# Optimization experiments

Hardware: AMD Instinct MI355X
Metric: run time of the kernel (lower is better)

The kernel has to match this reference:

```python
import jax, jax.numpy as jnp
import numpy as np

N = 100000          # total nodes
F = 128             # in_features
B = 1000            # number of graphs
NPG = 100           # nodes per graph (contiguous)
DEG = 16            # avg degree
E = B * NPG * DEG   # total edges (intra-graph)
K_RATIO = 0.8
KNUM = max(1, int(K_RATIO * NPG))  # nodes kept per graph = 80


def setup_inputs() -> dict:
    key = jax.random.key(0)
    k1, k2, k3, k4 = jax.random.split(key, 4)
    x = jax.random.normal(k1, (N, F), dtype=jnp.float32)
    # intra-graph random edges: offset each block of NPG*DEG edges by its graph's base node id
    offs = (jnp.arange(E, dtype=jnp.int32) // (NPG * DEG)) * NPG
    src = jax.random.randint(k2, (E,), 0, NPG, dtype=jnp.int32) + offs
    dst = jax.random.randint(k3, (E,), 0, NPG, dtype=jnp.int32) + offs
    edge_index = jnp.stack([src, dst], axis=0)
    batch = (jnp.arange(N, dtype=jnp.int32) // NPG).astype(jnp.int32)
    limit = float(np.sqrt(6.0 / (F + 1)))  # xavier_uniform for (F,1)
    theta_att = jax.random.uniform(k4, (F, 1), dtype=jnp.float32, minval=-limit, maxval=limit)
    return {"x": x, "edge_index": edge_index, "batch": batch, "theta_att": theta_att}


def reference(x, edge_index, batch, theta_att):
    num_nodes = x.shape[0]
    # add self loops with weight 1
    loops = jnp.arange(num_nodes, dtype=edge_index.dtype)
    row = jnp.concatenate([edge_index[0], loops])
    col = jnp.concatenate([edge_index[1], loops])
    w = jnp.ones(row.shape[0], dtype=x.dtype)
    # symmetric degree normalization (degree counted over row, as in torch code)
    deg = jax.ops.segment_sum(w, row, num_segments=num_nodes)
    dis = jnp.where(deg > 0, jax.lax.rsqrt(deg), jnp.zeros((), x.dtype))
    norm = dis[row] * w * dis[col]
    # scatter-add: agg[dst] += x[src] * norm
    agg = jax.ops.segment_sum(x[row] * norm[:, None], col, num_segments=num_nodes)
    z = (agg @ theta_att)[:, 0]                     # (N,)
    # per-graph top-k: graphs are contiguous and equal-sized -> reshape
    zb = z.reshape(B, NPG)
    _, pos = jax.lax.top_k(zb, KNUM)                # (B, KNUM) positions within each graph
    pos = jnp.sort(pos, axis=1)                     # global sort of keep_idx == per-graph sort here
    keep = (pos + jnp.arange(B, dtype=pos.dtype)[:, None] * NPG).reshape(-1)  # (B*KNUM,)
    scale = jax.nn.sigmoid(z[keep])[:, None]
    x_new = x[keep] * scale                         # (B*KNUM, F)
    batch_new = batch[keep]
    # subgraph with relabeled nodes; dropped edges padded with -1 (fixed shape for jit)
    node_mask = jnp.zeros(num_nodes, dtype=bool).at[keep].set(True)
    new_id = jnp.cumsum(node_mask.astype(jnp.int32)) - 1
    emask = node_mask[edge_index[0]] & node_mask[edge_index[1]]
    edge_index_new = jnp.where(emask[None, :], new_id[edge_index], -1)
    return x_new, edge_index_new, batch_new
```

## Files before the change

### kernel.cpp

```cpp
#include <hip/hip_runtime.h>


#define NPG   100
#define EPG   1600
#define KNUM  80
#define FDIM  128
#define BT    512
#define GPB   2
#define NF4   (NPG * FDIM / 4)
#define NE4   (EPG / 4)
#define NCH   (NF4 / BT)
#define NREM  (NF4 - NCH * BT)
#define PSTR  33

struct Smem {
    int4   edge4[NE4];
    int    cnt[8][NPG];
    double part[NPG * PSTR];
    double dis[NPG];
    double a[NPG];
    double zp[8][NPG];
    double z[NPG];
    unsigned long long mask7[8];
    int    newid[NPG];
    float  scalen[NPG];
};

__device__ __forceinline__
void process_graph(Smem& sm, int g, int tid, int wave, int lane, float4 th,
                   const float4 (&v)[NCH], float4 vR, int4 es, int4 ed,
                   float* __restrict__ out, int E_total, int out_x_elems)
{
    const int  base = g * NPG;
    const bool hasE = tid < NE4;
    const bool hasR = tid < NREM;
    int* sh_edge = (int*)sm.edge4;

    {
        int*    cw = sm.cnt[wave];
        double* zw = sm.zp[wave];
        for (int i = lane; i < NPG; i += 64) { cw[i] = 0; zw[i] = 0.0; }
    }

    int4 p;
    if (hasE) {
        int4 s4 = es, d4 = ed;
        s4.x -= base; s4.y -= base; s4.z -= base; s4.w -= base;
        d4.x -= base; d4.y -= base; d4.z -= base; d4.w -= base;
        p.x = s4.x | (d4.x << 16); p.y = s4.y | (d4.y << 16);
        p.z = s4.z | (d4.z << 16); p.w = s4.w | (d4.w << 16);
        sm.edge4[tid] = p;
        int* cw = sm.cnt[wave];
        atomicAdd(&cw[s4.x], 1); atomicAdd(&cw[s4.y], 1);
        atomicAdd(&cw[s4.z], 1); atomicAdd(&cw[s4.w], 1);
    }

    #pragma unroll
    for (int i = 0; i < NCH; ++i) {
        int idx = i * BT + tid;
        double dp = (double)v[i].x * th.x + (double)v[i].y * th.y
                  + (double)v[i].z * th.z + (double)v[i].w * th.w;
        sm.part[idx + (idx >> 5)] = dp;
    }
    if (hasR) {
        int idx = NCH * BT + tid;
        double dp = (double)vR.x * th.x + (double)vR.y * th.y
                  + (double)vR.z * th.z + (double)vR.w * th.w;
        sm.part[idx + (idx >> 5)] = dp;
    }
    __syncthreads();

    if (tid < 4 * NPG) {
        const int n = tid >> 2, q = tid & 3;
        const double* pr = sm.part + n * PSTR + q * 8;
        double s = ((pr[0] + pr[1]) + (pr[2] + pr[3]))
                 + ((pr[4] + pr[5]) + (pr[6] + pr[7]));
        s += __shfl_xor(s, 1, 64);
        s += __shfl_xor(s, 2, 64);
        if (q == 0) {
            int deg = 1 + sm.cnt[0][n] + sm.cnt[1][n] + sm.cnt[2][n]
                        + sm.cnt[3][n] + sm.cnt[4][n] + sm.cnt[5][n]
                        + sm.cnt[6][n] + sm.cnt[7][n];
            double dis = 1.0 / sqrt((double)deg);
            sm.dis[n] = dis;
            sm.a[n]   = s * dis;
        }
    }
    __syncthreads();

    {
        double* zw = sm.zp[wave];
        for (int j = tid; j < EPG; j += BT) {
            int e = sh_edge[j];
            atomicAdd(&zw[e >> 16], sm.a[e & 0xffff]);
        }
    }
    __syncthreads();

    if (tid < NPG) {
        double zi = sm.a[tid]
                  + sm.zp[0][tid] + sm.zp[1][tid] + sm.zp[2][tid] + sm.zp[3][tid]
                  + sm.zp[4][tid] + sm.zp[5][tid] + sm.zp[6][tid] + sm.zp[7][tid];
        sm.z[tid] = zi * sm.dis[tid];
        sm.newid[tid] = -1;
    }
    __syncthreads();

    const bool rk = tid < 4 * NPG;
    const int  n2 = tid >> 2;
    int r = 0;
    double zn = 0.0;
    if (rk) {
        zn = sm.z[n2];
        const int j0 = (tid & 3) * 25;
        for (int j = j0; j < j0 + 25; ++j) {
            double zj = sm.z[j];
            r += (int)((zj > zn) | ((zj == zn) & (j < n2)));
        }
    }
    r += __shfl_xor(r, 1, 64);
    r += __shfl_xor(r, 2, 64);
    const bool lead = rk && ((tid & 3) == 0) && (r < KNUM);
    unsigned long long m = __ballot(lead);
    if (lane == 0) sm.mask7[wave] = m;
    __syncthreads();

    if (lead) {
        int before = __popcll(m & ((1ull << lane) - 1ull));
        for (int w2 = 0; w2 < wave; ++w2) before += __popcll(sm.mask7[w2]);
        int row = g * KNUM + before;
        sm.newid[n2]  = row;
        sm.scalen[n2] = 1.0f / (1.0f + __expf(-(float)zn));
        out[(size_t)out_x_elems + 2 * (size_t)E_total + row] = (float)g;
    }
    __syncthreads();

    float4* outx = (float4*)out;
    #pragma unroll
    for (int i = 0; i < NCH; ++i) {
        int idx = i * BT + tid;
        int nid = sm.newid[idx >> 5];
        if (nid >= 0) {
            float sc = sm.scalen[idx >> 5];
            float4 o;
            o.x = v[i].x * sc; o.y = v[i].y * sc;
            o.z = v[i].z * sc; o.w = v[i].w * sc;
            outx[(size_t)nid * 32 + (idx & 31)] = o;
        }
    }
    if (hasR) {
        int idx = NCH * BT + tid;
        int nid = sm.newid[idx >> 5];
        if (nid >= 0) {
            float sc = sm.scalen[idx >> 5];
            float4 o;
            o.x = vR.x * sc; o.y = vR.y * sc;
            o.z = vR.z * sc; o.w = vR.w * sc;
            outx[(size_t)nid * 32 + (idx & 31)] = o;
        }
    }

    float* e0 = out + out_x_elems;
    float* e1 = e0 + E_total;
    if (hasE) {
        float4 o0, o1;
        {
            int a_ = sm.newid[p.x & 0xffff], b_ = sm.newid[p.x >> 16];
            bool vv = (a_ >= 0) && (b_ >= 0);
            o0.x = vv ? (float)a_ : -1.0f; o1.x = vv ? (float)b_ : -1.0f;
        }
        {
            int a_ = sm.newid[p.y & 0xffff], b_ = sm.newid[p.y >> 16];
            bool vv = (a_ >= 0) && (b_ >= 0);
            o0.y = vv ? (float)a_ : -1.0f; o1.y = vv ? (float)b_ : -1.0f;
        }
        {
            int a_ = sm.newid[p.z & 0xffff], b_ = sm.newid[p.z >> 16];
            bool vv = (a_ >= 0) && (b_ >= 0);
            o0.z = vv ? (float)a_ : -1.0f; o1.z = vv ? (float)b_ : -1.0f;
        }
        {
            int a_ = sm.newid[p.w & 0xffff], b_ = sm.newid[p.w >> 16];
            bool vv = (a_ >= 0) && (b_ >= 0);
            o0.w = vv ? (float)a_ : -1.0f; o1.w = vv ? (float)b_ : -1.0f;
        }
        ((float4*)e0)[(size_t)g * NE4 + tid] = o0;
        ((float4*)e1)[(size_t)g * NE4 + tid] = o1;
    }
}

__global__ __launch_bounds__(BT, 4)
void sagpool_fused7(const float* __restrict__ x,
                    const int*   __restrict__ ei,
                    const float* __restrict__ theta,
                    float* __restrict__ out,
                    int E_total, int out_x_elems, int n_graphs)
{
    __shared__ Smem sm;
    const int tid  = threadIdx.x;
    const int wave = tid >> 6;
    const int lane = tid & 63;
    const int gA   = blockIdx.x * GPB;
    const int gB   = gA + 1;
    const bool hasE = tid < NE4;
    const bool hasR = tid < NREM;

    const float4 th = ((const float4*)theta)[lane & 31];

    int4 esA, edA, esB, edB;
    float4 vA[NCH], vB[NCH], vRA, vRB;

    if (hasE) {
        esA = ((const int4*)(ei + (size_t)gA * EPG))[tid];
        edA = ((const int4*)(ei + (size_t)E_total + (size_t)gA * EPG))[tid];
    }
    {
        const float4* xb4 = (const float4*)(x + (size_t)gA * NPG * FDIM);
        #pragma unroll
        for (int i = 0; i < NCH; ++i) vA[i] = xb4[i * BT + tid];
        if (hasR) vRA = xb4[NCH * BT + tid];
    }
    const bool doB = gB < n_graphs;
    if (doB) {
        if (hasE) {
            esB = ((const int4*)(ei + (size_t)gB * EPG))[tid];
            edB = ((const int4*)(ei + (size_t)E_total + (size_t)gB * EPG))[tid];
        }
        const float4* xb4 = (const float4*)(x + (size_t)gB * NPG * FDIM);
        #pragma unroll
        for (int i = 0; i < NCH; ++i) vB[i] = xb4[i * BT + tid];
        if (hasR) vRB = xb4[NCH * BT + tid];
    }

    process_graph(sm, gA, tid, wave, lane, th, vA, vRA, esA, edA,
                  out, E_total, out_x_elems);
    if (doB)
        process_graph(sm, gB, tid, wave, lane, th, vB, vRB, esB, edB,
                      out, E_total, out_x_elems);
}

extern "C" void kernel_launch(void* const* d_in, const int* in_sizes, int n_in,
                              void* d_out, int out_size, void* d_ws, size_t ws_size,
                              hipStream_t stream)
{
    const float* x     = (const float*)d_in[0];
    const int*   ei    = (const int*)d_in[1];
    const float* theta = (const float*)d_in[3];
    float* out = (float*)d_out;

    const int N = in_sizes[0] / FDIM;
    const int E = in_sizes[1] / 2;
    const int B = N / NPG;
    const int out_x_elems = B * KNUM * FDIM;
    const int nb = (B + GPB - 1) / GPB;

    sagpool_fused7<<<dim3(nb), dim3(BT), 0, stream>>>(x, ei, theta, out,
                                                      E, out_x_elems, B);
}
```

Before: 129.7 us.

## Prefetch second graph's features into LDS via async global_load_lds during first graph

Instead of holding both graphs' feature rows in registers, the kernel keeps only graph A in registers and streams graph B's features directly into a 51KB LDS buffer with global_load_lds while graph A is processed. The per-node dot-product partials are pre-reduced with lane shuffles, shrinking the partial array and the reduction step. Barriers are replaced with a variant that waits only on LDS counters so the async prefetch is not drained at each sync. This cuts register pressure but raises LDS use per block, which may reduce occupancy. The prefetch also relies on the barrier before graph B to make the global_load_lds data visible.

```diff
diff --git a/kernel.cpp b/kernel.cpp
--- a/kernel.cpp
+++ b/kernel.cpp
@@ -6,17 +6,17 @@
 #define KNUM  80
 #define FDIM  128
 #define BT    512
-#define GPB   2
 #define NF4   (NPG * FDIM / 4)
 #define NE4   (EPG / 4)
 #define NCH   (NF4 / BT)
 #define NREM  (NF4 - NCH * BT)
-#define PSTR  33
+#define P8    9
 
 struct Smem {
+    alignas(16) float xB[NPG * FDIM];
     int4   edge4[NE4];
     int    cnt[8][NPG];
-    double part[NPG * PSTR];
+    double part[NPG * P8];
     double dis[NPG];
     double a[NPG];
     double zp[8][NPG];
@@ -26,9 +26,20 @@
     float  scalen[NPG];
 };
 
+typedef __attribute__((address_space(1))) const unsigned int gu32;
+typedef __attribute__((address_space(3))) unsigned int lu32;
+
+__device__ __forceinline__ void bar_nodrain() {
+    asm volatile("s_waitcnt lgkmcnt(0)" ::: "memory");
+    __builtin_amdgcn_s_barrier();
+    asm volatile("" ::: "memory");
+}
+
+template<bool FROMLDS, bool PF>
 __device__ __forceinline__
 void process_graph(Smem& sm, int g, int tid, int wave, int lane, float4 th,
-                   const float4 (&v)[NCH], float4 vR, int4 es, int4 ed,
+                   float4 (&v)[NCH], float4& vR, int4 es, int4 ed,
+                   const float4* pfsrc,
                    float* __restrict__ out, int E_total, int out_x_elems)
 {
     const int  base = g * NPG;
@@ -55,38 +66,56 @@
         atomicAdd(&cw[s4.z], 1); atomicAdd(&cw[s4.w], 1);
     }
 
+    const float4* xl = (const float4*)sm.xB;
     #pragma unroll
     for (int i = 0; i < NCH; ++i) {
         int idx = i * BT + tid;
+        if (FROMLDS) v[i] = xl[idx];
         double dp = (double)v[i].x * th.x + (double)v[i].y * th.y
                   + (double)v[i].z * th.z + (double)v[i].w * th.w;
-        sm.part[idx + (idx >> 5)] = dp;
+        dp += __shfl_xor(dp, 1, 64);
+        dp += __shfl_xor(dp, 2, 64);
+        if ((lane & 3) == 0)
+            sm.part[(idx >> 5) * P8 + ((idx & 31) >> 2)] = dp;
     }
     if (hasR) {
         int idx = NCH * BT + tid;
+        if (FROMLDS) vR = xl[idx];
         double dp = (double)vR.x * th.x + (double)vR.y * th.y
                   + (double)vR.z * th.z + (double)vR.w * th.w;
-        sm.part[idx + (idx >> 5)] = dp;
-    }
-    __syncthreads();
-
-    if (tid < 4 * NPG) {
-        const int n = tid >> 2, q = tid & 3;
-        const double* pr = sm.part + n * PSTR + q * 8;
+        dp += __shfl_xor(dp, 1, 64);
+        dp += __shfl_xor(dp, 2, 64);
+        if ((lane & 3) == 0)
+            sm.part[(idx >> 5) * P8 + ((idx & 31) >> 2)] = dp;
+    }
+
+    if (PF) {
+        #pragma unroll
+        for (int i = 0; i < NCH; ++i) {
+            int idx = i * BT + tid;
+            __builtin_amdgcn_global_load_lds((gu32*)(pfsrc + idx),
+                (lu32*)(sm.xB + (size_t)(i * BT + wave * 64) * 4), 16, 0, 0);
+        }
+        if (wave < 2) {
+            int idx = NCH * BT + tid;
+            __builtin_amdgcn_global_load_lds((gu32*)(pfsrc + idx),
+                (lu32*)(sm.xB + (size_t)(NCH * BT + wave * 64) * 4), 16, 0, 0);
+        }
+    }
+    bar_nodrain();
+
+    if (tid < NPG) {
+        const double* pr = sm.part + tid * P8;
         double s = ((pr[0] + pr[1]) + (pr[2] + pr[3]))
                  + ((pr[4] + pr[5]) + (pr[6] + pr[7]));
-        s += __shfl_xor(s, 1, 64);
-        s += __shfl_xor(s, 2, 64);
-        if (q == 0) {
-            int deg = 1 + sm.cnt[0][n] + sm.cnt[1][n] + sm.cnt[2][n]
-                        + sm.cnt[3][n] + sm.cnt[4][n] + sm.cnt[5][n]
-                        + sm.cnt[6][n] + sm.cnt[7][n];
-            double dis = 1.0 / sqrt((double)deg);
-            sm.dis[n] = dis;
-            sm.a[n]   = s * dis;
-        }
-    }
-    __syncthreads();
+        int deg = 1 + sm.cnt[0][tid] + sm.cnt[1][tid] + sm.cnt[2][tid]
+                    + sm.cnt[3][tid] + sm.cnt[4][tid] + sm.cnt[5][tid]
+                    + sm.cnt[6][tid] + sm.cnt[7][tid];
+        double dis = 1.0 / sqrt((double)deg);
+        sm.dis[tid] = dis;
+        sm.a[tid]   = s * dis;
+    }
+    bar_nodrain();
 
     {
         double* zw = sm.zp[wave];
@@ -95,7 +124,7 @@
             atomicAdd(&zw[e >> 16], sm.a[e & 0xffff]);
         }
     }
-    __syncthreads();
+    bar_nodrain();
 
     if (tid < NPG) {
         double zi = sm.a[tid]
@@ -104,7 +133,7 @@
         sm.z[tid] = zi * sm.dis[tid];
         sm.newid[tid] = -1;
     }
-    __syncthreads();
+    bar_nodrain();
 
     const bool rk = tid < 4 * NPG;
     const int  n2 = tid >> 2;
@@ -123,7 +152,7 @@
     const bool lead = rk && ((tid & 3) == 0) && (r < KNUM);
     unsigned long long m = __ballot(lead);
     if (lane == 0) sm.mask7[wave] = m;
-    __syncthreads();
+    bar_nodrain();
 
     if (lead) {
         int before = __popcll(m & ((1ull << lane) - 1ull));
@@ -133,7 +162,7 @@
         sm.scalen[n2] = 1.0f / (1.0f + __expf(-(float)zn));
         out[(size_t)out_x_elems + 2 * (size_t)E_total + row] = (float)g;
     }
-    __syncthreads();
+    bar_nodrain();
 
     float4* outx = (float4*)out;
     #pragma unroll
@@ -190,7 +219,7 @@
 }
 
 __global__ __launch_bounds__(BT, 4)
-void sagpool_fused7(const float* __restrict__ x,
+void sagpool_fused8(const float* __restrict__ x,
                     const int*   __restrict__ ei,
                     const float* __restrict__ theta,
                     float* __restrict__ out,
@@ -200,43 +229,38 @@
     const int tid  = threadIdx.x;
     const int wave = tid >> 6;
     const int lane = tid & 63;
-    const int gA   = blockIdx.x * GPB;
+    const int gA   = blockIdx.x * 2;
     const int gB   = gA + 1;
     const bool hasE = tid < NE4;
     const bool hasR = tid < NREM;
+    const bool doB  = gB < n_graphs;
 
     const float4 th = ((const float4*)theta)[lane & 31];
 
-    int4 esA, edA, esB, edB;
-    float4 vA[NCH], vB[NCH], vRA, vRB;
-
+    int4 esA = {0,0,0,0}, edA = {0,0,0,0}, esB = {0,0,0,0}, edB = {0,0,0,0};
     if (hasE) {
         esA = ((const int4*)(ei + (size_t)gA * EPG))[tid];
         edA = ((const int4*)(ei + (size_t)E_total + (size_t)gA * EPG))[tid];
-    }
-    {
-        const float4* xb4 = (const float4*)(x + (size_t)gA * NPG * FDIM);
-        #pragma unroll
-        for (int i = 0; i < NCH; ++i) vA[i] = xb4[i * BT + tid];
-        if (hasR) vRA = xb4[NCH * BT + tid];
-    }
-    const bool doB = gB < n_graphs;
-    if (doB) {
-        if (hasE) {
+        if (doB) {
             esB = ((const int4*)(ei + (size_t)gB * EPG))[tid];
             edB = ((const int4*)(ei + (size_t)E_total + (size_t)gB * EPG))[tid];
         }
-        const float4* xb4 = (const float4*)(x + (size_t)gB * NPG * FDIM);
-        #pragma unroll
-        for (int i = 0; i < NCH; ++i) vB[i] = xb4[i * BT + tid];
-        if (hasR) vRB = xb4[NCH * BT + tid];
-    }
-
-    process_graph(sm, gA, tid, wave, lane, th, vA, vRA, esA, edA,
-                  out, E_total, out_x_elems);
-    if (doB)
-        process_graph(sm, gB, tid, wave, lane, th, vB, vRB, esB, edB,
-                      out, E_total, out_x_elems);
+    }
+    float4 v[NCH];
+    float4 vR = {0.f, 0.f, 0.f, 0.f};
+    const float4* xA = (const float4*)(x + (size_t)gA * NPG * FDIM);
+    const float4* xB = (const float4*)(x + (size_t)gB * NPG * FDIM);
+    #pragma unroll
+    for (int i = 0; i < NCH; ++i) v[i] = xA[i * BT + tid];
+    if (hasR) vR = xA[NCH * BT + tid];
+
+    process_graph<false, true>(sm, gA, tid, wave, lane, th, v, vR, esA, edA,
+                               xB, out, E_total, out_x_elems);
+    if (doB) {
+        __syncthreads();
+        process_graph<true, false>(sm, gB, tid, wave, lane, th, v, vR, esB, edB,
+                                   nullptr, out, E_total, out_x_elems);
+    }
 }
 
 extern "C" void kernel_launch(void* const* d_in, const int* in_sizes, int n_in,
@@ -252,8 +276,8 @@
     const int E = in_sizes[1] / 2;
     const int B = N / NPG;
     const int out_x_elems = B * KNUM * FDIM;
-    const int nb = (B + GPB - 1) / GPB;
-
-    sagpool_fused7<<<dim3(nb), dim3(BT), 0, stream>>>(x, ei, theta, out,
+    const int nb = (B + 1) / 2;
+
+    sagpool_fused8<<<dim3(nb), dim3(BT), 0, stream>>>(x, ei, theta, out,
                                                       E, out_x_elems, B);
 }
```

After: 112.5 us. 1.15x faster.

## Process one graph per block with shuffle-reduced dot products and smaller shared memory

Applied to the files above, without the earlier changes.

Each block now handles a single graph instead of two, with 1000 blocks and launch bounds raised to allow 8 blocks per CU. The per-row dot product against theta is pre-reduced across 8 lanes with shuffles before the shared-memory write, so the part buffer shrinks and one thread per node finishes the sum, merging the degree and partial-sum steps. The z scatter uses 4 partial accumulators instead of 8 to cut shared memory. The aim is more parallelism and occupancy and fewer barriers, at the cost of extra shuffles and more atomic contention per accumulator.

```diff
diff --git a/kernel.cpp b/kernel.cpp
--- a/kernel.cpp
+++ b/kernel.cpp
@@ -6,43 +6,87 @@
 #define KNUM  80
 #define FDIM  128
 #define BT    512
-#define GPB   2
 #define NF4   (NPG * FDIM / 4)
 #define NE4   (EPG / 4)
 #define NCH   (NF4 / BT)
 #define NREM  (NF4 - NCH * BT)
-#define PSTR  33
+#define P4    5
 
 struct Smem {
     int4   edge4[NE4];
     int    cnt[8][NPG];
-    double part[NPG * PSTR];
+    double part[NPG * P4];
     double dis[NPG];
     double a[NPG];
-    double zp[8][NPG];
+    double zp[4][NPG];
     double z[NPG];
     unsigned long long mask7[8];
     int    newid[NPG];
     float  scalen[NPG];
 };
 
-__device__ __forceinline__
-void process_graph(Smem& sm, int g, int tid, int wave, int lane, float4 th,
-                   const float4 (&v)[NCH], float4 vR, int4 es, int4 ed,
-                   float* __restrict__ out, int E_total, int out_x_elems)
+__global__ __launch_bounds__(BT, 8)
+void sagpool_fused11(const float* __restrict__ x,
+                     const int*   __restrict__ ei,
+                     const float* __restrict__ theta,
+                     float* __restrict__ out,
+                     int E_total, int out_x_elems)
 {
-    const int  base = g * NPG;
+    __shared__ Smem sm;
+    const int g    = blockIdx.x;
+    const int tid  = threadIdx.x;
+    const int wave = tid >> 6;
+    const int lane = tid & 63;
+    const int base = g * NPG;
     const bool hasE = tid < NE4;
     const bool hasR = tid < NREM;
     int* sh_edge = (int*)sm.edge4;
 
+    const float4 th = ((const float4*)theta)[lane & 31];
+
+    float4 v[NCH];
+    float4 vR = {0.f, 0.f, 0.f, 0.f};
+    const float4* xb4 = (const float4*)(x + (size_t)base * FDIM);
+    #pragma unroll
+    for (int i = 0; i < NCH; ++i) v[i] = xb4[i * BT + tid];
+    if (hasR) vR = xb4[NCH * BT + tid];
+
+    int4 es = {0,0,0,0}, ed = {0,0,0,0};
+    if (hasE) {
+        es = ((const int4*)(ei + (size_t)g * EPG))[tid];
+        ed = ((const int4*)(ei + (size_t)E_total + (size_t)g * EPG))[tid];
+    }
+
     {
-        int*    cw = sm.cnt[wave];
-        double* zw = sm.zp[wave];
-        for (int i = lane; i < NPG; i += 64) { cw[i] = 0; zw[i] = 0.0; }
-    }
-
-    int4 p;
+        int* cw = sm.cnt[wave];
+        for (int i = lane; i < NPG; i += 64) cw[i] = 0;
+        double* zw = sm.zp[wave >> 1];
+        for (int i = lane; i < NPG; i += 64) zw[i] = 0.0;
+    }
+
+    #pragma unroll
+    for (int i = 0; i < NCH; ++i) {
+        int idx = i * BT + tid;
+        double dp = (double)v[i].x * th.x + (double)v[i].y * th.y
+                  + (double)v[i].z * th.z + (double)v[i].w * th.w;
+        dp += __shfl_xor(dp, 1, 64);
+        dp += __shfl_xor(dp, 2, 64);
+        dp += __shfl_xor(dp, 4, 64);
+        if ((lane & 7) == 0)
+            sm.part[(idx >> 5) * P4 + ((lane & 31) >> 3)] = dp;
+    }
+    if (hasR) {
+        int idx = NCH * BT + tid;
+        double dp = (double)vR.x * th.x + (double)vR.y * th.y
+                  + (double)vR.z * th.z + (double)vR.w * th.w;
+        dp += __shfl_xor(dp, 1, 64);
+        dp += __shfl_xor(dp, 2, 64);
+        dp += __shfl_xor(dp, 4, 64);
+        if ((lane & 7) == 0)
+            sm.part[(idx >> 5) * P4 + ((lane & 31) >> 3)] = dp;
+    }
+
+    int4 p = {0,0,0,0};
     if (hasE) {
         int4 s4 = es, d4 = ed;
         s4.x -= base; s4.y -= base; s4.z -= base; s4.w -= base;
@@ -54,42 +98,22 @@
         atomicAdd(&cw[s4.x], 1); atomicAdd(&cw[s4.y], 1);
         atomicAdd(&cw[s4.z], 1); atomicAdd(&cw[s4.w], 1);
     }
-
-    #pragma unroll
-    for (int i = 0; i < NCH; ++i) {
-        int idx = i * BT + tid;
-        double dp = (double)v[i].x * th.x + (double)v[i].y * th.y
-                  + (double)v[i].z * th.z + (double)v[i].w * th.w;
-        sm.part[idx + (idx >> 5)] = dp;
-    }
-    if (hasR) {
-        int idx = NCH * BT + tid;
-        double dp = (double)vR.x * th.x + (double)vR.y * th.y
-                  + (double)vR.z * th.z + (double)vR.w * th.w;
-        sm.part[idx + (idx >> 5)] = dp;
-    }
-    __syncthreads();
-
-    if (tid < 4 * NPG) {
-        const int n = tid >> 2, q = tid & 3;
-        const double* pr = sm.part + n * PSTR + q * 8;
-        double s = ((pr[0] + pr[1]) + (pr[2] + pr[3]))
-                 + ((pr[4] + pr[5]) + (pr[6] + pr[7]));
-        s += __shfl_xor(s, 1, 64);
-        s += __shfl_xor(s, 2, 64);
-        if (q == 0) {
-            int deg = 1 + sm.cnt[0][n] + sm.cnt[1][n] + sm.cnt[2][n]
-                        + sm.cnt[3][n] + sm.cnt[4][n] + sm.cnt[5][n]
-                        + sm.cnt[6][n] + sm.cnt[7][n];
-            double dis = 1.0 / sqrt((double)deg);
-            sm.dis[n] = dis;
-            sm.a[n]   = s * dis;
-        }
+    __syncthreads();
+
+    if (tid < NPG) {
+        const double* pr = sm.part + tid * P4;
+        double s = (pr[0] + pr[1]) + (pr[2] + pr[3]);
+        int deg = 1 + sm.cnt[0][tid] + sm.cnt[1][tid] + sm.cnt[2][tid]
+                    + sm.cnt[3][tid] + sm.cnt[4][tid] + sm.cnt[5][tid]
+                    + sm.cnt[6][tid] + sm.cnt[7][tid];
+        double dis = 1.0 / sqrt((double)deg);
+        sm.dis[tid] = dis;
+        sm.a[tid]   = s * dis;
     }
     __syncthreads();
 
     {
-        double* zw = sm.zp[wave];
+        double* zw = sm.zp[wave >> 1];
         for (int j = tid; j < EPG; j += BT) {
             int e = sh_edge[j];
             atomicAdd(&zw[e >> 16], sm.a[e & 0xffff]);
@@ -99,8 +123,8 @@
 
     if (tid < NPG) {
         double zi = sm.a[tid]
-                  + sm.zp[0][tid] + sm.zp[1][tid] + sm.zp[2][tid] + sm.zp[3][tid]
-                  + sm.zp[4][tid] + sm.zp[5][tid] + sm.zp[6][tid] + sm.zp[7][tid];
+                  + (sm.zp[0][tid] + sm.zp[1][tid])
+                  + (sm.zp[2][tid] + sm.zp[3][tid]);
         sm.z[tid] = zi * sm.dis[tid];
         sm.newid[tid] = -1;
     }
@@ -113,6 +137,7 @@
     if (rk) {
         zn = sm.z[n2];
         const int j0 = (tid & 3) * 25;
+        #pragma unroll 5
         for (int j = j0; j < j0 + 25; ++j) {
             double zj = sm.z[j];
             r += (int)((zj > zn) | ((zj == zn) & (j < n2)));
@@ -139,9 +164,10 @@
     #pragma unroll
     for (int i = 0; i < NCH; ++i) {
         int idx = i * BT + tid;
-        int nid = sm.newid[idx >> 5];
+        int row = idx >> 5;
+        int nid = sm.newid[row];
         if (nid >= 0) {
-            float sc = sm.scalen[idx >> 5];
+            float sc = sm.scalen[row];
             float4 o;
             o.x = v[i].x * sc; o.y = v[i].y * sc;
             o.z = v[i].z * sc; o.w = v[i].w * sc;
@@ -150,9 +176,10 @@
     }
     if (hasR) {
         int idx = NCH * BT + tid;
-        int nid = sm.newid[idx >> 5];
+        int row = idx >> 5;
+        int nid = sm.newid[row];
         if (nid >= 0) {
-            float sc = sm.scalen[idx >> 5];
+            float sc = sm.scalen[row];
             float4 o;
             o.x = vR.x * sc; o.y = vR.y * sc;
             o.z = vR.z * sc; o.w = vR.w * sc;
@@ -160,9 +187,9 @@
         }
     }
 
-    float* e0 = out + out_x_elems;
-    float* e1 = e0 + E_total;
     if (hasE) {
+        float* e0 = out + out_x_elems;
+        float* e1 = e0 + E_total;
         float4 o0, o1;
         {
             int a_ = sm.newid[p.x & 0xffff], b_ = sm.newid[p.x >> 16];
@@ -187,56 +214,6 @@
         ((float4*)e0)[(size_t)g * NE4 + tid] = o0;
         ((float4*)e1)[(size_t)g * NE4 + tid] = o1;
     }
-}
-
-__global__ __launch_bounds__(BT, 4)
-void sagpool_fused7(const float* __restrict__ x,
-                    const int*   __restrict__ ei,
-                    const float* __restrict__ theta,
-                    float* __restrict__ out,
-                    int E_total, int out_x_elems, int n_graphs)
-{
-    __shared__ Smem sm;
-    const int tid  = threadIdx.x;
-    const int wave = tid >> 6;
-    const int lane = tid & 63;
-    const int gA   = blockIdx.x * GPB;
-    const int gB   = gA + 1;
-    const bool hasE = tid < NE4;
-    const bool hasR = tid < NREM;
-
-    const float4 th = ((const float4*)theta)[lane & 31];
-
-    int4 esA, edA, esB, edB;
-    float4 vA[NCH], vB[NCH], vRA, vRB;
-
-    if (hasE) {
-        esA = ((const int4*)(ei + (size_t)gA * EPG))[tid];
-        edA = ((const int4*)(ei + (size_t)E_total + (size_t)gA * EPG))[tid];
-    }
-    {
-        const float4* xb4 = (const float4*)(x + (size_t)gA * NPG * FDIM);
-        #pragma unroll
-        for (int i = 0; i < NCH; ++i) vA[i] = xb4[i * BT + tid];
-        if (hasR) vRA = xb4[NCH * BT + tid];
-    }
-    const bool doB = gB < n_graphs;
-    if (doB) {
-        if (hasE) {
-            esB = ((const int4*)(ei + (size_t)gB * EPG))[tid];
-            edB = ((const int4*)(ei + (size_t)E_total + (size_t)gB * EPG))[tid];
-        }
-        const float4* xb4 = (const float4*)(x + (size_t)gB * NPG * FDIM);
-        #pragma unroll
-        for (int i = 0; i < NCH; ++i) vB[i] = xb4[i * BT + tid];
-        if (hasR) vRB = xb4[NCH * BT + tid];
-    }
-
-    process_graph(sm, gA, tid, wave, lane, th, vA, vRA, esA, edA,
-                  out, E_total, out_x_elems);
-    if (doB)
-        process_graph(sm, gB, tid, wave, lane, th, vB, vRB, esB, edB,
-                      out, E_total, out_x_elems);
 }
 
 extern "C" void kernel_launch(void* const* d_in, const int* in_sizes, int n_in,
@@ -252,8 +229,7 @@
     const int E = in_sizes[1] / 2;
     const int B = N / NPG;
     const int out_x_elems = B * KNUM * FDIM;
-    const int nb = (B + GPB - 1) / GPB;
-
-    sagpool_fused7<<<dim3(nb), dim3(BT), 0, stream>>>(x, ei, theta, out,
-                                                      E, out_x_elems, B);
+
+    sagpool_fused11<<<dim3(B), dim3(BT), 0, stream>>>(x, ei, theta, out,
+                                                      E, out_x_elems);
 }
```

Result: faster. 109.5 us (-15.6%).
